# Optimization experiments

Measured on AMD Instinct MI355X. Metric: run time of the kernel, lower is better.

Reference implementation:

```python
import jax, jax.numpy as jnp
import numpy as np
import math

B, S, D = 16, 577, 768          # batch, seq (24*24 grid + 1 cls), in_dim=att_dim
H, HD = 12, 64                  # heads, head_dim
GRID = 24                       # height = width; S = GRID*GRID + rpe_skip
RATIO = 1.9
ALPHA, BETA, GAMMA = 1.0 * RATIO, 2.0 * RATIO, 8.0 * RATIO
BETA_INT = int(BETA)            # 3
NUM_BUCKETS = (2 * BETA_INT + 1) ** 2 + 1  # 49 product buckets + 1 extra for skip (cls) = 50


def _piecewise_index(d):
    # iRPE piecewise bucket index (numpy, static). d: integer offsets.
    d = d.astype(np.float64)
    ad = np.abs(d)
    log_part = ALPHA + np.log(np.maximum(ad, 1e-9) / ALPHA) / math.log(GAMMA / ALPHA) * (BETA - ALPHA)
    y_out = np.sign(d) * np.clip(np.round(log_part), None, BETA)
    idx = np.where(ad <= ALPHA, np.round(d), y_out)
    return np.trunc(idx).astype(np.int64)  # torch .to(int) truncates toward zero


def make_rp_bucket():
    # 2D 'product' method bucket ids with skip=1 (cls token -> extra bucket)
    ii, jj = np.meshgrid(np.arange(GRID), np.arange(GRID), indexing='ij')
    pos = np.stack([ii.ravel(), jj.ravel()], axis=-1)          # (L,2)
    diff = pos[:, None, :] - pos[None, :, :]                    # (L,L,2)
    Sb = 2 * BETA_INT + 1
    r = _piecewise_index(diff[..., 0]) + BETA_INT               # [0, 2*beta_int]
    c = _piecewise_index(diff[..., 1]) + BETA_INT
    pid = r * Sb + c                                            # [0, 48]
    L = GRID * GRID
    bucket = np.full((L + 1, L + 1), NUM_BUCKETS - 1, dtype=np.int32)
    bucket[1:, 1:] = pid
    return jnp.asarray(bucket)


def setup_inputs() -> dict:
    key = jax.random.key(0)
    k1, k2, k3 = jax.random.split(key, 3)
    x = jax.random.normal(k1, (B, S, D), dtype=jnp.float32)
    w_qkv = jax.random.normal(k2, (3 * D, D), dtype=jnp.float32) * 0.02   # torch Linear weight (out,in)
    rpe_table = jax.random.normal(k3, (HD, NUM_BUCKETS), dtype=jnp.float32) * 0.02  # shared-head contextual table
    rp_bucket = make_rp_bucket()                                # (S,S) int32
    return {"x": x, "w_qkv": w_qkv, "rpe_table": rpe_table, "rp_bucket": rp_bucket}


def reference(x, w_qkv, rpe_table, rp_bucket):
    qkv = x @ w_qkv.T                                           # (B,S,3D)
    q, k, v = jnp.split(qkv, 3, axis=-1)
    # Faithful to torch source: plain reshape (B,S,D)->(B,H,S,HD) (no transpose-split)
    scale = 1.0 / jnp.sqrt(jnp.asarray(HD, x.dtype))
    q = q.reshape(B, H, S, HD) * scale
    k = k.reshape(B, H, S, HD)
    v = v.reshape(B, H, S, HD)
    qk = jnp.einsum('bhid,bhjd->bhij', q, k)                    # (B,H,S,S)
    # contextual rpe_k: bias[b,h,i,j] = (q[b,h,i] . rpe_table[:, rp_bucket[i,j]])
    ctx = jnp.einsum('bhid,dc->bhic', q, rpe_table)             # (B,H,S,NUM_BUCKETS)
    idx = jnp.broadcast_to(rp_bucket[None, None].astype(jnp.int32), (B, H, S, S))
    bias = jnp.take_along_axis(ctx, idx, axis=-1)               # (B,H,S,S)
    att = jax.nn.softmax(qk + bias, axis=-1)
    out = jnp.einsum('bhij,bhjd->bhid', att, v)                 # (B,H,S,HD)
    y = out.transpose(0, 2, 1, 3).reshape(B, S, D)              # out_proj is Identity (out_dim==att_dim)
    return y
```

## Files before the change

kernel.cpp:

```cpp
#include <hip/hip_runtime.h>

constexpr int BN_  = 16;
constexpr int SN_  = 577;
constexpr int SP_  = 640;
constexpr int DN_  = 768;
constexpr int HN_  = 12;
constexpr int HD_  = 64;
constexpr int NB_  = 50;
constexpr int MR_  = BN_ * SN_;
constexpr int MRP_ = 73 * 128;
constexpr int NQ_  = 3 * DN_;
constexpr int BHS_ = BN_ * HN_ * SN_;
constexpr int SHD_ = SN_ * HD_;

constexpr int NBX_ = MRP_ * DN_ / 2048;
constexpr int NBW_ = NQ_ * DN_ / 2048;
constexpr int NRPX_ = 5 * 4 * 2 * 10 * 4 * 64;
constexpr int NBRX_ = NRPX_ / 256;

constexpr int QKV_WG_ = 18 * 73;

typedef __attribute__((ext_vector_type(8))) short short8;
typedef __attribute__((ext_vector_type(4))) float f32x4;

__device__ __forceinline__ short f2bf(float f) {
  union { float f; unsigned u; } v; v.f = f;
  unsigned r = (v.u + 0x7fffu + ((v.u >> 16) & 1u)) >> 16;
  return (short)r;
}

__device__ __forceinline__ float ex2(float x) {
  float r; asm("v_exp_f32 %0, %1" : "=v"(r) : "v"(x)); return r;
}

__device__ __forceinline__ unsigned cvtpk(float a, float b) {
  unsigned r; asm("v_cvt_pk_bf16_f32 %0, %1, %2" : "=v"(r) : "v"(a), "v"(b));
  return r;
}

__device__ __forceinline__ float bf2f(unsigned short u) {
  union { unsigned u; float f; } v; v.u = ((unsigned)u) << 16; return v.f;
}

__device__ __forceinline__ void gload16(const void* g, void* l) {
  __builtin_amdgcn_global_load_lds(
      (const __attribute__((address_space(1))) unsigned int*)g,
      (__attribute__((address_space(3))) unsigned int*)l, 16, 0, 0);
}

__launch_bounds__(256)
__global__ void prep_k(const float* __restrict__ x, short* __restrict__ xb,
                       const float* __restrict__ w, short* __restrict__ wb,
                       const int* __restrict__ rpb, unsigned* __restrict__ rpbX) {
  const int bid = blockIdx.x;
  const int t = threadIdx.x;
  if (bid < NBX_ + NBW_) {
    const float* src; short* dst; int n_src, i;
    if (bid < NBX_) { src = x; dst = xb; n_src = MR_ * DN_; i = (bid * 256 + t) * 8; }
    else { src = w; dst = wb; n_src = NQ_ * DN_; i = ((bid - NBX_) * 256 + t) * 8; }
    union { short8 v; short u[8]; } pk;
    if (i < n_src) {
      const float4 a = *(const float4*)(src + i);
      const float4 b = *(const float4*)(src + i + 4);
      pk.u[0] = f2bf(a.x); pk.u[1] = f2bf(a.y); pk.u[2] = f2bf(a.z); pk.u[3] = f2bf(a.w);
      pk.u[4] = f2bf(b.x); pk.u[5] = f2bf(b.y); pk.u[6] = f2bf(b.z); pk.u[7] = f2bf(b.w);
    } else {
#pragma unroll
      for (int j = 0; j < 8; ++j) pk.u[j] = 0;
    }
    *(short8*)(dst + i) = pk.v;
  } else {
    const int idx = (bid - NBX_ - NBW_) * 256 + t;
    if (idx >= NRPX_) return;
    const int lane = idx & 63, chunk = idx >> 6;
    const int nt = chunk & 3;
    const int jt = (chunk >> 2) % 10;
    const int rest = chunk / 40;
    const int s  = rest & 1;
    const int w4 = (rest >> 1) & 3;
    const int qt = rest >> 3;
    const int g = lane >> 4, ln = lane & 15;
    int row = qt * 128 + w4 * 32 + s * 16 + ln;
    if (row > SN_ - 1) row = SN_ - 1;
    const int j0 = jt * 64 + nt * 16 + 4 * g;
    union { unsigned u; uchar4 c; } pk;
    pk.c.x = (j0     < SN_) ? (unsigned char)rpb[row * SN_ + j0    ] : 0;
    pk.c.y = (j0 + 1 < SN_) ? (unsigned char)rpb[row * SN_ + j0 + 1] : 0;
    pk.c.z = (j0 + 2 < SN_) ? (unsigned char)rpb[row * SN_ + j0 + 2] : 0;
    pk.c.w = (j0 + 3 < SN_) ? (unsigned char)rpb[row * SN_ + j0 + 3] : 0;
    rpbX[idx] = pk.u;
  }
}

__launch_bounds__(256)
__global__ void qkv_mfma_k(const short* __restrict__ xb, const short* __restrict__ wb,
                           short* __restrict__ Qbf, short* __restrict__ Ksw,
                           short* __restrict__ Vbf) {
  __shared__ short SB[32768];
  const int t = threadIdx.x;
  const int w = t >> 6, lane = t & 63, g = lane >> 4, ln = lane & 15;
  const int wm = w >> 1, wn = w & 1;

  const int bid = blockIdx.x;
  const int xcd = bid & 7, li = bid >> 3;
  const int sid = (xcd < 2) ? xcd * 165 + li : 2 * 165 + (xcd - 2) * 164 + li;
  const int mi = sid / 18, ni = sid - mi * 18;
  const int m0 = mi * 128, n0 = ni * 128;

  const int rlo = lane >> 3;
  const int gu  = (lane & 7) ^ rlo;
  const short* ga[4]; const short* gb[4];
  int lOff[4];
#pragma unroll
  for (int q = 0; q < 4; ++q) {
    const int rl = w * 32 + q * 8 + rlo;
    ga[q] = xb + (size_t)(m0 + rl) * DN_ + gu * 8;
    gb[q] = wb + (size_t)(n0 + rl) * DN_ + gu * 8;
    lOff[q] = w * 2048 + q * 512;
  }

  f32x4 acc[4][4];
#pragma unroll
  for (int mt = 0; mt < 4; ++mt)
#pragma unroll
    for (int nt = 0; nt < 4; ++nt) acc[mt][nt] = (f32x4){0.f, 0.f, 0.f, 0.f};

#pragma unroll
  for (int q = 0; q < 4; ++q) {
    gload16(ga[q], SB + lOff[q]);
    gload16(gb[q], SB + 16384 + lOff[q]);
  }
#pragma unroll
  for (int q = 0; q < 4; ++q) {
    gload16(ga[q] + 64, SB + 8192 + lOff[q]);
    gload16(gb[q] + 64, SB + 16384 + 8192 + lOff[q]);
  }

  int cur = 0;
  for (int k0 = 0; k0 < DN_; k0 += 64) {
    if (k0 + 64 < DN_) {
      asm volatile("s_waitcnt vmcnt(8)" ::: "memory");
    } else {
      asm volatile("s_waitcnt vmcnt(0)" ::: "memory");
    }
    __builtin_amdgcn_sched_barrier(0);
    __builtin_amdgcn_s_barrier();
    __builtin_amdgcn_sched_barrier(0);

    const short* Ac = SB + cur * 8192;
    const short* Bc = SB + 16384 + cur * 8192;
#pragma unroll
    for (int kc = 0; kc < 2; ++kc) {
      short8 af[4], bf[4];
#pragma unroll
      for (int mt = 0; mt < 4; ++mt) {
        const int row = wm * 64 + mt * 16 + ln;
        const int u = (kc * 4 + g) ^ (row & 7);
        af[mt] = *(const short8*)&Ac[row * 64 + u * 8];
      }
#pragma unroll
      for (int nt = 0; nt < 4; ++nt) {
        const int row = wn * 64 + nt * 16 + ln;
        const int u = (kc * 4 + g) ^ (row & 7);
        bf[nt] = *(const short8*)&Bc[row * 64 + u * 8];
      }
#pragma unroll
      for (int mt = 0; mt < 4; ++mt)
#pragma unroll
        for (int nt = 0; nt < 4; ++nt)
          acc[mt][nt] = __builtin_amdgcn_mfma_f32_16x16x32_bf16(af[mt], bf[nt], acc[mt][nt], 0, 0, 0);
    }

    __builtin_amdgcn_s_barrier();
    __builtin_amdgcn_sched_barrier(0);

    if (k0 + 128 < DN_) {
      const int nb = cur * 8192;
#pragma unroll
      for (int q = 0; q < 4; ++q) {
        gload16(ga[q] + k0 + 128, SB + nb + lOff[q]);
        gload16(gb[q] + k0 + 128, SB + 16384 + nb + lOff[q]);
      }
    }
    cur ^= 1;
  }

  const int wbase = w * 4608;
  const int nw0  = n0 + wn * 64;
  const int secg = nw0 / DN_;
  const int cbw  = nw0 - secg * DN_;
  const float QSC = 0.18033688011112042f;
#pragma unroll
  for (int mt = 0; mt < 4; ++mt)
#pragma unroll
    for (int nt = 0; nt < 4; ++nt)
#pragma unroll
      for (int r = 0; r < 4; ++r) {
        float v = acc[mt][nt][r];
        if (secg == 0) v *= QSC;
        SB[wbase + (mt * 16 + 4 * g + r) * 72 + nt * 16 + ln] = f2bf(v);
      }
  const int gm = m0 + wm * 64 + lane;
  if (gm < MR_) {
    const int bb = gm / SN_;
    const int ss = gm - bb * SN_;
    const int pr = ss * DN_ + cbw;
    const int hh = pr / SHD_;
    const int ii = (pr - hh * SHD_) >> 6;
    const size_t ro = (size_t)(bb * HN_ + hh);
    const short* src = SB + wbase + lane * 72;
    if (secg == 0) {
      short* dst = Qbf + (ro * SN_ + ii) * 64;
#pragma unroll
      for (int u = 0; u < 8; ++u)
        *(short8*)(dst + u * 8) = *(const short8*)(src + u * 8);
    } else if (secg == 1) {
      short* dst = Ksw + (ro * SP_ + ii) * 64;
      const int sw = ii & 7;
#pragma unroll
      for (int u = 0; u < 8; ++u)
        *(short8*)(dst + (u ^ sw) * 8) = *(const short8*)(src + u * 8);
    } else {
      short* dst = Vbf + (ro * SP_ + ii) * 64;
#pragma unroll
      for (int u = 0; u < 8; ++u)
        *(short8*)(dst + u * 8) = *(const short8*)(src + u * 8);
    }
  }
}

__launch_bounds__(256)
__global__ void vtr_k(const short* __restrict__ Vbf, short* __restrict__ Vtsw) {
  __shared__ short T[64][72];
  const int t = threadIdx.x;
  const int jt = blockIdx.x, bh = blockIdx.y;
  const int j0 = jt * 64;
  {
    const int r = t >> 2, c0 = (t & 3) * 16;
    const short* src = Vbf + ((size_t)bh * SP_ + j0 + r) * 64 + c0;
    *(short8*)&T[r][c0]     = *(const short8*)(src);
    *(short8*)&T[r][c0 + 8] = *(const short8*)(src + 8);
  }
  __syncthreads();
  const int d = t >> 2;
  short* dst = Vtsw + ((size_t)bh * 64 + d) * SP_;
  const int sw = (d & 7) << 3;
#pragma unroll
  for (int e = 0; e < 4; ++e) {
    const int jl = (t & 3) * 16 + e * 4;
    const int jg = j0 + jl;
    short4 v;
    v.x = (jg + 0 < SN_) ? T[jl + 0][d] : (short)0;
    v.y = (jg + 1 < SN_) ? T[jl + 1][d] : (short)0;
    v.z = (jg + 2 < SN_) ? T[jl + 2][d] : (short)0;
    v.w = (jg + 3 < SN_) ? T[jl + 3][d] : (short)0;
    const int oq = (jg >> 2) & 7;
    const int pq = ((oq & 3) << 1) | (oq >> 2);
    const int p  = (jg & ~31) | (pq << 2);
    *(short4*)&dst[p ^ sw] = v;
  }
}

__launch_bounds__(256)
__global__ void attn_k(const short* __restrict__ Qbf, const short* __restrict__ Ksw,
                       const short* __restrict__ Vtsw, const float* __restrict__ rpe,
                       const unsigned* __restrict__ rpbX, float* __restrict__ y) {
  __shared__ short Kt[4096];
  __shared__ short Vt[4096];
  __shared__ unsigned short ctxs[4][32][53];
  short (*Rp)[64] = (short (*)[64])ctxs;

  const int t = threadIdx.x;
  const int w = t >> 6, lane = t & 63, g = lane >> 4, ln = lane & 15;
  const int wg = blockIdx.x;
  const int xcd = wg & 7, idx = wg >> 3;
  const int qt = idx % 5;
  const int bh = (idx / 5) * 8 + xcd;
  const int b = bh / HN_, h = bh - b * HN_;
  const int i0 = qt * 128;
  const size_t rb = (size_t)bh * SN_;
  const short* Kbh = Ksw + (size_t)bh * SP_ * 64;
  const short* Vbh = Vtsw + (size_t)bh * 64 * SP_;

  const int tK = t * 8;
  const int vRow = t >> 3, vCol = (t & 7) * 8;

  const unsigned* rpB = rpbX + qt * 20480 + w * 5120 + lane;

  short8 kr0, kr1, vr0, vr1;
  kr0 = *(const short8*)(Kbh + tK);
  kr1 = *(const short8*)(Kbh + 2048 + tK);
  vr0 = *(const short8*)(Vbh + (size_t)vRow * SP_ + vCol);
  vr1 = *(const short8*)(Vbh + (size_t)(32 + vRow) * SP_ + vCol);

  for (int e = t; e < 64 * 64; e += 256) {
    const int c = e >> 6, d = e & 63;
    Rp[c][d] = (c < NB_) ? f2bf(rpe[d * NB_ + c]) : (short)0;
  }

  short8 qf[2][2];
#pragma unroll
  for (int s = 0; s < 2; ++s) {
    int row = i0 + 32 * w + 16 * s + ln; if (row > SN_ - 1) row = SN_ - 1;
    const short* qp = Qbf + (rb + row) * 64;
    qf[s][0] = *(const short8*)(qp + 8 * g);
    qf[s][1] = *(const short8*)(qp + 32 + 8 * g);
  }

  __syncthreads();

  f32x4 accC[2][4];
#pragma unroll
  for (int s = 0; s < 2; ++s)
#pragma unroll
    for (int ct = 0; ct < 4; ++ct) accC[s][ct] = (f32x4){0.f, 0.f, 0.f, 0.f};
#pragma unroll
  for (int kc = 0; kc < 2; ++kc) {
#pragma unroll
    for (int ct = 0; ct < 4; ++ct) {
      const short8 rf = *(const short8*)&Rp[ct * 16 + ln][kc * 32 + 8 * g];
      accC[0][ct] = __builtin_amdgcn_mfma_f32_16x16x32_bf16(qf[0][kc], rf, accC[0][ct], 0, 0, 0);
      accC[1][ct] = __builtin_amdgcn_mfma_f32_16x16x32_bf16(qf[1][kc], rf, accC[1][ct], 0, 0, 0);
    }
  }
  __syncthreads();

#pragma unroll
  for (int s = 0; s < 2; ++s)
#pragma unroll
    for (int ct = 0; ct < 4; ++ct) {
      const int c = ct * 16 + ln;
      if (c < 53) {
#pragma unroll
        for (int r = 0; r < 4; ++r)
          ctxs[w][16 * s + 4 * g + r][c] = (unsigned short)f2bf(accC[s][ct][r]);
      }
    }

  float m0s = -3e38f, m1s = -3e38f, l0s = 0.f, l1s = 0.f;
  f32x4 accO[2][4];
#pragma unroll
  for (int s = 0; s < 2; ++s)
#pragma unroll
    for (int dt = 0; dt < 4; ++dt) accO[s][dt] = (f32x4){0.f, 0.f, 0.f, 0.f};

  const int swv = (ln & 7) << 3;

  for (int jt = 0; jt < 10; ++jt) {
    __syncthreads();
    *(short8*)&Kt[tK]        = kr0;
    *(short8*)&Kt[2048 + tK] = kr1;
    *(short8*)&Vt[tK]        = vr0;
    *(short8*)&Vt[2048 + tK] = vr1;
    __syncthreads();

    unsigned rpg[2][4];
#pragma unroll
    for (int s = 0; s < 2; ++s)
#pragma unroll
      for (int nt = 0; nt < 4; ++nt)
        rpg[s][nt] = rpB[s * 2560 + jt * 256 + nt * 64];

    if (jt < 9) {
      const int jn = jt * 64 + 64;
      kr0 = *(const short8*)(Kbh + (size_t)jn * 64 + tK);
      kr1 = *(const short8*)(Kbh + (size_t)jn * 64 + 2048 + tK);
      vr0 = *(const short8*)(Vbh + (size_t)vRow * SP_ + jn + vCol);
      vr1 = *(const short8*)(Vbh + (size_t)(32 + vRow) * SP_ + jn + vCol);
    }

    f32x4 accS[2][4];
#pragma unroll
    for (int s = 0; s < 2; ++s)
#pragma unroll
      for (int nt = 0; nt < 4; ++nt) accS[s][nt] = (f32x4){0.f, 0.f, 0.f, 0.f};
    __builtin_amdgcn_s_setprio(1);
#pragma unroll
    for (int kc = 0; kc < 2; ++kc) {
      const int cb = (kc * 32 + 8 * g) ^ swv;
#pragma unroll
      for (int nt = 0; nt < 4; ++nt) {
        const short8 kf = *(const short8*)&Kt[(nt * 16 + ln) * 64 + cb];
        accS[0][nt] = __builtin_amdgcn_mfma_f32_16x16x32_bf16(kf, qf[0][kc], accS[0][nt], 0, 0, 0);
        accS[1][nt] = __builtin_amdgcn_mfma_f32_16x16x32_bf16(kf, qf[1][kc], accS[1][nt], 0, 0, 0);
      }
    }
    __builtin_amdgcn_s_setprio(0);

    short8 pf[2][2];
#pragma unroll
    for (int s = 0; s < 2; ++s) {
      const unsigned short* cbase = &ctxs[w][16 * s + ln][0];
      float pv[4][4];
#pragma unroll
      for (int nt = 0; nt < 4; ++nt) {
        union { unsigned u; uchar4 c; } bk; bk.u = rpg[s][nt];
        pv[nt][0] = accS[s][nt][0] + bf2f(cbase[bk.c.x]);
        pv[nt][1] = accS[s][nt][1] + bf2f(cbase[bk.c.y]);
        pv[nt][2] = accS[s][nt][2] + bf2f(cbase[bk.c.z]);
        pv[nt][3] = accS[s][nt][3] + bf2f(cbase[bk.c.w]);
      }
      if (jt == 9) {
#pragma unroll
        for (int nt = 0; nt < 4; ++nt) {
          const int jb = jt * 64 + nt * 16 + 4 * g;
#pragma unroll
          for (int r = 0; r < 4; ++r)
            if (jb + r >= SN_) pv[nt][r] = -3e38f;
        }
      }

      float& m = (s == 0) ? m0s : m1s;
      float& l = (s == 0) ? l0s : l1s;

      float mq[4];
#pragma unroll
      for (int nt = 0; nt < 4; ++nt)
        mq[nt] = fmaxf(fmaxf(pv[nt][0], pv[nt][1]), fmaxf(pv[nt][2], pv[nt][3]));
      float mx = fmaxf(fmaxf(mq[0], mq[1]), fmaxf(mq[2], mq[3]));
      mx = fmaxf(mx, __shfl_xor(mx, 16));
      mx = fmaxf(mx, __shfl_xor(mx, 32));

      if (__any(mx > m + 8.f)) {
        const float mnew = fmaxf(m, mx);
        const float sc = ex2(m - mnew);
        float scr[4];
#pragma unroll
        for (int r = 0; r < 4; ++r) scr[r] = __shfl(sc, 4 * g + r);
#pragma unroll
        for (int dt = 0; dt < 4; ++dt)
#pragma unroll
          for (int r = 0; r < 4; ++r) accO[s][dt][r] *= scr[r];
        l *= sc;
        m = mnew;
      }

#pragma unroll
      for (int nt = 0; nt < 4; ++nt)
#pragma unroll
        for (int r = 0; r < 4; ++r)
          pv[nt][r] = ex2(pv[nt][r] - m);
      float sq[4];
#pragma unroll
      for (int nt = 0; nt < 4; ++nt)
        sq[nt] = (pv[nt][0] + pv[nt][1]) + (pv[nt][2] + pv[nt][3]);
      float sum = (sq[0] + sq[1]) + (sq[2] + sq[3]);
      sum += __shfl_xor(sum, 16);
      sum += __shfl_xor(sum, 32);
      l += sum;

#pragma unroll
      for (int kc = 0; kc < 2; ++kc) {
        union { short8 v; unsigned wd[4]; } pk;
        pk.wd[0] = cvtpk(pv[2 * kc][0],     pv[2 * kc][1]);
        pk.wd[1] = cvtpk(pv[2 * kc][2],     pv[2 * kc][3]);
        pk.wd[2] = cvtpk(pv[2 * kc + 1][0], pv[2 * kc + 1][1]);
        pk.wd[3] = cvtpk(pv[2 * kc + 1][2], pv[2 * kc + 1][3]);
        pf[s][kc] = pk.v;
      }
    }

    __builtin_amdgcn_s_setprio(1);
#pragma unroll
    for (int kc = 0; kc < 2; ++kc) {
      const int cb = (kc * 32 + 8 * g) ^ swv;
#pragma unroll
      for (int dt = 0; dt < 4; ++dt) {
        const short8 vf = *(const short8*)&Vt[(dt * 16 + ln) * 64 + cb];
        accO[0][dt] = __builtin_amdgcn_mfma_f32_16x16x32_bf16(pf[0][kc], vf, accO[0][dt], 0, 0, 0);
        accO[1][dt] = __builtin_amdgcn_mfma_f32_16x16x32_bf16(pf[1][kc], vf, accO[1][dt], 0, 0, 0);
      }
    }
    __builtin_amdgcn_s_setprio(0);
  }

#pragma unroll
  for (int s = 0; s < 2; ++s) {
    const float lv = (s == 0) ? l0s : l1s;
    float linv[4];
#pragma unroll
    for (int r = 0; r < 4; ++r) linv[r] = 1.f / __shfl(lv, 4 * g + r);
#pragma unroll
    for (int r = 0; r < 4; ++r) {
      const int i = i0 + 32 * w + 16 * s + 4 * g + r;
      if (i >= SN_) continue;
      float* yp = y + ((size_t)b * SN_ + i) * DN_ + h * HD_ + ln;
#pragma unroll
      for (int dt = 0; dt < 4; ++dt) yp[dt * 16] = accO[s][dt][r] * linv[r];
    }
  }
}

extern "C" void kernel_launch(void* const* d_in, const int* in_sizes, int n_in,
                              void* d_out, int out_size, void* d_ws, size_t ws_size,
                              hipStream_t stream) {
  const float* x   = (const float*)d_in[0];
  const float* w   = (const float*)d_in[1];
  const float* rpe = (const float*)d_in[2];
  const int*   rpb = (const int*)d_in[3];
  float* y = (float*)d_out;

  short* xb   = (short*)d_ws;
  short* wb   = xb + (size_t)MRP_ * DN_;
  short* Qbf  = wb + (size_t)NQ_ * DN_;
  short* Ksw  = Qbf + (size_t)BHS_ * HD_;
  short* Vbf  = Ksw + (size_t)BN_ * HN_ * SP_ * 64;
  short* Vtsw = Vbf + (size_t)BN_ * HN_ * SP_ * 64;
  unsigned* rpbX = (unsigned*)(Vtsw + (size_t)BN_ * HN_ * 64 * SP_);

  prep_k<<<dim3(NBX_ + NBW_ + NBRX_), 256, 0, stream>>>(x, xb, w, wb, rpb, rpbX);
  qkv_mfma_k<<<dim3(QKV_WG_), 256, 0, stream>>>(xb, wb, Qbf, Ksw, Vbf);
  vtr_k<<<dim3(10, BN_ * HN_), 256, 0, stream>>>(Vbf, Vtsw);
  attn_k<<<dim3(960), 256, 0, stream>>>(Qbf, Ksw, Vtsw, rpe, rpbX, y);
}
```

Before: 134.5 us.

## Split attention key range across two workgroups and merge with a combine kernel

Each query tile's attention is now split into two halves of the key/value sequence, so twice as many workgroups are launched. Each half writes an unnormalized bf16 partial output plus its running max and sum into reused workspace buffers. A new combine kernel rescales and merges the two partials into the final fp32 output. This adds parallelism for better CU fill, at the cost of recomputing the per-tile setup (Q and rpe context), an extra launch and memory round trip, and bf16 rounding of the partial outputs.

```diff
diff --git a/kernel.cpp b/kernel.cpp
--- a/kernel.cpp
+++ b/kernel.cpp
@@ -264,7 +264,9 @@
 __launch_bounds__(256)
 __global__ void attn_k(const short* __restrict__ Qbf, const short* __restrict__ Ksw,
                        const short* __restrict__ Vtsw, const float* __restrict__ rpe,
-                       const unsigned* __restrict__ rpbX, float* __restrict__ y) {
+                       const unsigned* __restrict__ rpbX,
+                       short* __restrict__ Oa, short* __restrict__ Ob,
+                       float* __restrict__ ml) {
   __shared__ short Kt[4096];
   __shared__ short Vt[4096];
   __shared__ unsigned short ctxs[4][32][53];
@@ -274,10 +276,11 @@
   const int w = t >> 6, lane = t & 63, g = lane >> 4, ln = lane & 15;
   const int wg = blockIdx.x;
   const int xcd = wg & 7, idx = wg >> 3;
-  const int qt = idx % 5;
-  const int bh = (idx / 5) * 8 + xcd;
-  const int b = bh / HN_, h = bh - b * HN_;
+  const int sub = idx % 10;
+  const int qt = sub % 5, half = sub / 5;
+  const int bh = (idx / 10) * 8 + xcd;
   const int i0 = qt * 128;
+  const int jt0 = half * 5;
   const size_t rb = (size_t)bh * SN_;
   const short* Kbh = Ksw + (size_t)bh * SP_ * 64;
   const short* Vbh = Vtsw + (size_t)bh * 64 * SP_;
@@ -288,10 +291,10 @@
   const unsigned* rpB = rpbX + qt * 20480 + w * 5120 + lane;
 
   short8 kr0, kr1, vr0, vr1;
-  kr0 = *(const short8*)(Kbh + tK);
-  kr1 = *(const short8*)(Kbh + 2048 + tK);
-  vr0 = *(const short8*)(Vbh + (size_t)vRow * SP_ + vCol);
-  vr1 = *(const short8*)(Vbh + (size_t)(32 + vRow) * SP_ + vCol);
+  kr0 = *(const short8*)(Kbh + (size_t)(jt0 * 64) * 64 + tK);
+  kr1 = *(const short8*)(Kbh + (size_t)(jt0 * 64) * 64 + 2048 + tK);
+  vr0 = *(const short8*)(Vbh + (size_t)vRow * SP_ + jt0 * 64 + vCol);
+  vr1 = *(const short8*)(Vbh + (size_t)(32 + vRow) * SP_ + jt0 * 64 + vCol);
 
   for (int e = t; e < 64 * 64; e += 256) {
     const int c = e >> 6, d = e & 63;
@@ -346,7 +349,7 @@
 
   const int swv = (ln & 7) << 3;
 
-  for (int jt = 0; jt < 10; ++jt) {
+  for (int jt = jt0; jt < jt0 + 5; ++jt) {
     __syncthreads();
     *(short8*)&Kt[tK]        = kr0;
     *(short8*)&Kt[2048 + tK] = kr1;
@@ -361,7 +364,7 @@
       for (int nt = 0; nt < 4; ++nt)
         rpg[s][nt] = rpB[s * 2560 + jt * 256 + nt * 64];
 
-    if (jt < 9) {
+    if (jt < jt0 + 4) {
       const int jn = jt * 64 + 64;
       kr0 = *(const short8*)(Kbh + (size_t)jn * 64 + tK);
       kr1 = *(const short8*)(Kbh + (size_t)jn * 64 + 2048 + tK);
@@ -474,21 +477,61 @@
     __builtin_amdgcn_s_setprio(0);
   }
 
+  float* mArr = ml + (size_t)half * 2 * BHS_;
+  float* lArr = mArr + BHS_;
+  short* Oh = half ? Ob : Oa;
 #pragma unroll
   for (int s = 0; s < 2; ++s) {
+    const float mv = (s == 0) ? m0s : m1s;
     const float lv = (s == 0) ? l0s : l1s;
-    float linv[4];
-#pragma unroll
-    for (int r = 0; r < 4; ++r) linv[r] = 1.f / __shfl(lv, 4 * g + r);
+    const int ri = i0 + 32 * w + 16 * s + ln;
+    if (g == 0 && ri < SN_) {
+      mArr[rb + ri] = mv;
+      lArr[rb + ri] = lv;
+    }
 #pragma unroll
     for (int r = 0; r < 4; ++r) {
       const int i = i0 + 32 * w + 16 * s + 4 * g + r;
       if (i >= SN_) continue;
-      float* yp = y + ((size_t)b * SN_ + i) * DN_ + h * HD_ + ln;
-#pragma unroll
-      for (int dt = 0; dt < 4; ++dt) yp[dt * 16] = accO[s][dt][r] * linv[r];
-    }
-  }
+      short* op = Oh + (rb + i) * 64 + ln;
+#pragma unroll
+      for (int dt = 0; dt < 4; ++dt) op[dt * 16] = f2bf(accO[s][dt][r]);
+    }
+  }
+}
+
+__launch_bounds__(256)
+__global__ void cmb_k(const short* __restrict__ Oa, const short* __restrict__ Ob,
+                      const float* __restrict__ ml, float* __restrict__ y) {
+  const int gtid = blockIdx.x * 256 + threadIdx.x;
+  const int row = gtid >> 3;
+  if (row >= BHS_) return;
+  const int dseg = (gtid & 7) * 8;
+  const float ma_ = ml[row],            la_ = ml[BHS_ + row];
+  const float mb_ = ml[2 * BHS_ + row], lb_ = ml[3 * BHS_ + row];
+  const float M  = fmaxf(ma_, mb_);
+  const float ea = ex2(ma_ - M), eb = ex2(mb_ - M);
+  const float inv = 1.f / (la_ * ea + lb_ * eb);
+  const float fa = ea * inv, fb = eb * inv;
+  union { short8 v; short u[8]; } oa, ob;
+  oa.v = *(const short8*)(Oa + (size_t)row * 64 + dseg);
+  ob.v = *(const short8*)(Ob + (size_t)row * 64 + dseg);
+  const int bh = row / SN_;
+  const int i  = row - bh * SN_;
+  const int b  = bh / HN_;
+  const int h  = bh - b * HN_;
+  float* yp = y + ((size_t)b * SN_ + i) * DN_ + h * HD_ + dseg;
+  float4 o0, o1;
+  o0.x = bf2f((unsigned short)oa.u[0]) * fa + bf2f((unsigned short)ob.u[0]) * fb;
+  o0.y = bf2f((unsigned short)oa.u[1]) * fa + bf2f((unsigned short)ob.u[1]) * fb;
+  o0.z = bf2f((unsigned short)oa.u[2]) * fa + bf2f((unsigned short)ob.u[2]) * fb;
+  o0.w = bf2f((unsigned short)oa.u[3]) * fa + bf2f((unsigned short)ob.u[3]) * fb;
+  o1.x = bf2f((unsigned short)oa.u[4]) * fa + bf2f((unsigned short)ob.u[4]) * fb;
+  o1.y = bf2f((unsigned short)oa.u[5]) * fa + bf2f((unsigned short)ob.u[5]) * fb;
+  o1.z = bf2f((unsigned short)oa.u[6]) * fa + bf2f((unsigned short)ob.u[6]) * fb;
+  o1.w = bf2f((unsigned short)oa.u[7]) * fa + bf2f((unsigned short)ob.u[7]) * fb;
+  *(float4*)yp       = o0;
+  *(float4*)(yp + 4) = o1;
 }
 
 extern "C" void kernel_launch(void* const* d_in, const int* in_sizes, int n_in,
@@ -508,8 +551,13 @@
   short* Vtsw = Vbf + (size_t)BN_ * HN_ * SP_ * 64;
   unsigned* rpbX = (unsigned*)(Vtsw + (size_t)BN_ * HN_ * 64 * SP_);
 
+  short* Oa  = xb;
+  short* Ob  = Vbf;
+  float* ml  = (float*)wb;
+
   prep_k<<<dim3(NBX_ + NBW_ + NBRX_), 256, 0, stream>>>(x, xb, w, wb, rpb, rpbX);
   qkv_mfma_k<<<dim3(QKV_WG_), 256, 0, stream>>>(xb, wb, Qbf, Ksw, Vbf);
   vtr_k<<<dim3(10, BN_ * HN_), 256, 0, stream>>>(Vbf, Vtsw);
-  attn_k<<<dim3(960), 256, 0, stream>>>(Qbf, Ksw, Vtsw, rpe, rpbX, y);
-}
+  attn_k<<<dim3(1920), 256, 0, stream>>>(Qbf, Ksw, Vtsw, rpe, rpbX, Oa, Ob, ml);
+  cmb_k<<<dim3(BHS_ * 8 / 256), 256, 0, stream>>>(Oa, Ob, ml, y);
+}
```

Measured after the change: 158.4 us. 1.18x slower.
